# Performance work log

Hardware: AMD Instinct MI355X
Metric: run time of the kernel (lower is better)

Reference implementation:

```python
import jax, jax.numpy as jnp
import numpy as np

N, E = 50000, 800000
NODE_DIM, EDGE_DIM, HID, OUT = 128, 16, 256, 32
NEG_SLOPE = 0.2


def setup_inputs() -> dict:
    key = jax.random.key(0)
    ks = jax.random.split(key, 20)
    def p(k, shape, fan_in):
        return jax.random.normal(k, shape, dtype=jnp.float32) * (1.0 / np.sqrt(fan_in))
    inp = {
        'x': jax.random.normal(ks[0], (N, NODE_DIM), dtype=jnp.float32),
        'edge_index': jax.random.randint(ks[1], (2, E), 0, N, dtype=jnp.int32),
        'edge_attr': jax.random.normal(ks[2], (E, EDGE_DIM), dtype=jnp.float32),
        # layer 1: GATv2Conv(node_dim -> 256, edge_dim)
        'Wl1': p(ks[3], (NODE_DIM, HID), NODE_DIM), 'bl1': jnp.zeros((HID,), jnp.float32),
        'Wr1': p(ks[4], (NODE_DIM, HID), NODE_DIM), 'br1': jnp.zeros((HID,), jnp.float32),
        'We1': p(ks[5], (EDGE_DIM, HID), EDGE_DIM),
        'att1': p(ks[6], (HID,), HID), 'bias1': jnp.zeros((HID,), jnp.float32),
        # layer 2: GATv2Conv(256 -> 32, edge_dim)
        'Wl2': p(ks[7], (HID, OUT), HID), 'bl2': jnp.zeros((OUT,), jnp.float32),
        'Wr2': p(ks[8], (HID, OUT), HID), 'br2': jnp.zeros((OUT,), jnp.float32),
        'We2': p(ks[9], (EDGE_DIM, OUT), EDGE_DIM),
        'att2': p(ks[10], (OUT,), OUT), 'bias2': jnp.zeros((OUT,), jnp.float32),
    }
    return inp


def _gatv2_layer(x, src, dst, ea, Wl, bl, Wr, br, We, att, bias, n_nodes):
    # GATv2: e_ij = att . leaky_relu(Wl x_j + Wr x_i + We e_ij), softmax over j for each target i
    xl = x @ Wl + bl            # [N, C] source transform
    xr = x @ Wr + br            # [N, C] target transform
    ee = ea @ We                # [Etot, C]
    z = jax.nn.leaky_relu(xl[src] + xr[dst] + ee, NEG_SLOPE)  # [Etot, C]
    e = z @ att                 # [Etot]
    m = jax.ops.segment_max(e, dst, num_segments=n_nodes)
    m = jnp.where(jnp.isfinite(m), m, 0.0)
    a = jnp.exp(e - m[dst])
    s = jax.ops.segment_sum(a, dst, num_segments=n_nodes)
    alpha = a / (s[dst] + 1e-16)
    out = jax.ops.segment_sum(alpha[:, None] * xl[src], dst, num_segments=n_nodes)
    return out + bias


def reference(x, edge_index, edge_attr, Wl1, bl1, Wr1, br1, We1, att1, bias1,
              Wl2, bl2, Wr2, br2, We2, att2, bias2):
    n = x.shape[0]
    src, dst = edge_index[0], edge_index[1]
    # add_self_loops with fill_value='mean': self-loop attr = mean of incoming edge_attr
    deg = jax.ops.segment_sum(jnp.ones((src.shape[0],), x.dtype), dst, num_segments=n)
    loop_attr = jax.ops.segment_sum(edge_attr, dst, num_segments=n) / jnp.maximum(deg, 1.0)[:, None]
    ar = jnp.arange(n, dtype=src.dtype)
    src_a = jnp.concatenate([src, ar])
    dst_a = jnp.concatenate([dst, ar])
    ea = jnp.concatenate([edge_attr, loop_attr], axis=0)
    h = _gatv2_layer(x, src_a, dst_a, ea, Wl1, bl1, Wr1, br1, We1, att1, bias1, n)
    h = _gatv2_layer(h, src_a, dst_a, ea, Wl2, bl2, Wr2, br2, We2, att2, bias2, n)
    return h.mean(0)  # [OUT]
```

## Files before the change

kernel.cpp:

```cpp
#include <hip/hip_runtime.h>
#include <hip/hip_bf16.h>
#include <stdint.h>


#define NN 50000
#define NE 800000
#define DIN 128
#define DE 16
#define HID 256
#define OUTD 32
#define SLOPE 0.2f
#define CAP 64
#define FILLBLKS 3125

__global__ __launch_bounds__(256) void k_fill_xform1(
    const int* __restrict__ srcv, const int* __restrict__ dstv,
    int* __restrict__ deg, int2* __restrict__ es,
    const float* __restrict__ x, const float* __restrict__ Wl,
    const float* __restrict__ bl, const float* __restrict__ Wr,
    const float* __restrict__ br, float* __restrict__ xl, float* __restrict__ xr) {
  const int bid = blockIdx.x;
  if (bid < FILLBLKS) {
    int e = bid * 256 + threadIdx.x;
    if (e < NE) {
      int d = dstv[e];
      int p = atomicAdd(&deg[d], 1);
      if (p < CAP) es[(size_t)d * CAP + p] = make_int2(e, srcv[e]);
    }
    return;
  }
  const int c = threadIdx.x;
  const int r0 = (bid - FILLBLKS) * 16;
  float accl[16], accr[16];
#pragma unroll
  for (int r = 0; r < 16; ++r) { accl[r] = 0.f; accr[r] = 0.f; }
  const float* __restrict__ xb = x + (size_t)r0 * DIN;
#pragma unroll 4
  for (int k = 0; k < DIN; ++k) {
    const float wl = Wl[k * HID + c];
    const float wr = Wr[k * HID + c];
#pragma unroll
    for (int r = 0; r < 16; ++r) {
      const float xv = xb[r * DIN + k];
      accl[r] = fmaf(xv, wl, accl[r]);
      accr[r] = fmaf(xv, wr, accr[r]);
    }
  }
  const float blc = bl[c], brc = br[c];
#pragma unroll
  for (int r = 0; r < 16; ++r) {
    xl[(size_t)(r0 + r) * HID + c] = accl[r] + blc;
    xr[(size_t)(r0 + r) * HID + c] = accr[r] + brc;
  }
}


__global__ __launch_bounds__(256) void k_loopattr(
    const float* __restrict__ ea, const int* __restrict__ degv,
    const int2* __restrict__ es, float* __restrict__ loopat) {
  const int tid = threadIdx.x;
  const int lane = tid & 63;
  const int wid = tid >> 6;
  const int node = blockIdx.x * 4 + wid;
  const int grp = lane >> 4;
  const int ch = lane & 15;
  const int deg = degv[node];
  const int r0 = node * CAP, r1 = r0 + deg;

  float acc = 0.f;
  for (int j = r0 + grp; j < r1; j += 4) {
    const int e = es[j].x;
    acc += ea[(size_t)e * DE + ch];
  }
  acc += __shfl_xor(acc, 16, 64);
  acc += __shfl_xor(acc, 32, 64);
  if (grp == 0) {
    const float invd = 1.f / (float)(deg > 0 ? deg : 1);
    loopat[(size_t)node * DE + ch] = acc * invd;
  }
}


__global__ __launch_bounds__(256)
__attribute__((amdgpu_num_vgpr(64))) void k_edge1(
    const float* __restrict__ xl, const float* __restrict__ xr,
    const float* __restrict__ eattr, const float* __restrict__ loopat,
    const int* __restrict__ degv, const int2* __restrict__ es,
    const float* __restrict__ We, const float* __restrict__ att,
    const float* __restrict__ bias, float* __restrict__ hout) {
  const int tid = threadIdx.x;
  const int lane = tid & 63;
  const int wid = tid >> 6;
  const int node = blockIdx.x * 4 + wid;
  const int c0 = lane << 2;

  float we[DE][4];
#pragma unroll
  for (int k = 0; k < DE; ++k) {
    const float4 w4 = *(const float4*)(We + k * HID + c0);
    we[k][0] = w4.x; we[k][1] = w4.y; we[k][2] = w4.z; we[k][3] = w4.w;
  }
  const float4 attv = *(const float4*)(att + c0);
  const float4 xrv = *(const float4*)(xr + (size_t)node * HID + c0);
  const int r0 = node * CAP;
  const int r1 = r0 + degv[node];

  float ssum = 0.f;
  float a0 = 0.f, a1 = 0.f, a2 = 0.f, a3 = 0.f;

  auto pscore = [&](const float* __restrict__ eap, const float4 xs) -> float {
    const float4* __restrict__ eb = (const float4*)eap;
    const float4 A0 = eb[0], A1 = eb[1], A2 = eb[2], A3 = eb[3];
    float e0, e1, e2, e3;
    e0 = A0.x * we[0][0]; e1 = A0.x * we[0][1];
    e2 = A0.x * we[0][2]; e3 = A0.x * we[0][3];
    e0 = fmaf(A0.y, we[1][0], e0); e1 = fmaf(A0.y, we[1][1], e1);
    e2 = fmaf(A0.y, we[1][2], e2); e3 = fmaf(A0.y, we[1][3], e3);
    e0 = fmaf(A0.z, we[2][0], e0); e1 = fmaf(A0.z, we[2][1], e1);
    e2 = fmaf(A0.z, we[2][2], e2); e3 = fmaf(A0.z, we[2][3], e3);
    e0 = fmaf(A0.w, we[3][0], e0); e1 = fmaf(A0.w, we[3][1], e1);
    e2 = fmaf(A0.w, we[3][2], e2); e3 = fmaf(A0.w, we[3][3], e3);
    e0 = fmaf(A1.x, we[4][0], e0); e1 = fmaf(A1.x, we[4][1], e1);
    e2 = fmaf(A1.x, we[4][2], e2); e3 = fmaf(A1.x, we[4][3], e3);
    e0 = fmaf(A1.y, we[5][0], e0); e1 = fmaf(A1.y, we[5][1], e1);
    e2 = fmaf(A1.y, we[5][2], e2); e3 = fmaf(A1.y, we[5][3], e3);
    e0 = fmaf(A1.z, we[6][0], e0); e1 = fmaf(A1.z, we[6][1], e1);
    e2 = fmaf(A1.z, we[6][2], e2); e3 = fmaf(A1.z, we[6][3], e3);
    e0 = fmaf(A1.w, we[7][0], e0); e1 = fmaf(A1.w, we[7][1], e1);
    e2 = fmaf(A1.w, we[7][2], e2); e3 = fmaf(A1.w, we[7][3], e3);
    e0 = fmaf(A2.x, we[8][0], e0); e1 = fmaf(A2.x, we[8][1], e1);
    e2 = fmaf(A2.x, we[8][2], e2); e3 = fmaf(A2.x, we[8][3], e3);
    e0 = fmaf(A2.y, we[9][0], e0); e1 = fmaf(A2.y, we[9][1], e1);
    e2 = fmaf(A2.y, we[9][2], e2); e3 = fmaf(A2.y, we[9][3], e3);
    e0 = fmaf(A2.z, we[10][0], e0); e1 = fmaf(A2.z, we[10][1], e1);
    e2 = fmaf(A2.z, we[10][2], e2); e3 = fmaf(A2.z, we[10][3], e3);
    e0 = fmaf(A2.w, we[11][0], e0); e1 = fmaf(A2.w, we[11][1], e1);
    e2 = fmaf(A2.w, we[11][2], e2); e3 = fmaf(A2.w, we[11][3], e3);
    e0 = fmaf(A3.x, we[12][0], e0); e1 = fmaf(A3.x, we[12][1], e1);
    e2 = fmaf(A3.x, we[12][2], e2); e3 = fmaf(A3.x, we[12][3], e3);
    e0 = fmaf(A3.y, we[13][0], e0); e1 = fmaf(A3.y, we[13][1], e1);
    e2 = fmaf(A3.y, we[13][2], e2); e3 = fmaf(A3.y, we[13][3], e3);
    e0 = fmaf(A3.z, we[14][0], e0); e1 = fmaf(A3.z, we[14][1], e1);
    e2 = fmaf(A3.z, we[14][2], e2); e3 = fmaf(A3.z, we[14][3], e3);
    e0 = fmaf(A3.w, we[15][0], e0); e1 = fmaf(A3.w, we[15][1], e1);
    e2 = fmaf(A3.w, we[15][2], e2); e3 = fmaf(A3.w, we[15][3], e3);
    float z0 = xs.x + xrv.x + e0;
    float z1 = xs.y + xrv.y + e1;
    float z2 = xs.z + xrv.z + e2;
    float z3 = xs.w + xrv.w + e3;
    z0 = fmaxf(z0, SLOPE * z0);
    z1 = fmaxf(z1, SLOPE * z1);
    z2 = fmaxf(z2, SLOPE * z2);
    z3 = fmaxf(z3, SLOPE * z3);
    float p = z0 * attv.x;
    p = fmaf(z1, attv.y, p);
    p = fmaf(z2, attv.z, p);
    p = fmaf(z3, attv.w, p);
    return p;
  };

  auto upd = [&](float p, const float4 xs) {
    const float w = __expf(p);
    ssum += w;
    a0 = fmaf(w, xs.x, a0);
    a1 = fmaf(w, xs.y, a1);
    a2 = fmaf(w, xs.z, a2);
    a3 = fmaf(w, xs.w, a3);
  };

  int j = r0;
  for (; j + 4 <= r1; j += 4) {
    const int2 q0 = es[j], q1 = es[j + 1], q2 = es[j + 2], q3 = es[j + 3];
    const int s0i = __builtin_amdgcn_readfirstlane(q0.y);
    const int s1i = __builtin_amdgcn_readfirstlane(q1.y);
    const int s2i = __builtin_amdgcn_readfirstlane(q2.y);
    const int s3i = __builtin_amdgcn_readfirstlane(q3.y);
    const int e0i = __builtin_amdgcn_readfirstlane(q0.x);
    const int e1i = __builtin_amdgcn_readfirstlane(q1.x);
    const int e2i = __builtin_amdgcn_readfirstlane(q2.x);
    const int e3i = __builtin_amdgcn_readfirstlane(q3.x);
    const float4 xs0 = *(const float4*)(xl + (size_t)s0i * HID + c0);
    const float4 xs1 = *(const float4*)(xl + (size_t)s1i * HID + c0);
    const float4 xs2 = *(const float4*)(xl + (size_t)s2i * HID + c0);
    const float4 xs3 = *(const float4*)(xl + (size_t)s3i * HID + c0);
    float p0 = pscore(eattr + (size_t)e0i * DE, xs0);
    float p1 = pscore(eattr + (size_t)e1i * DE, xs1);
    float p2 = pscore(eattr + (size_t)e2i * DE, xs2);
    float p3 = pscore(eattr + (size_t)e3i * DE, xs3);
#pragma unroll
    for (int off = 32; off >= 1; off >>= 1) {
      p0 += __shfl_xor(p0, off, 64);
      p1 += __shfl_xor(p1, off, 64);
      p2 += __shfl_xor(p2, off, 64);
      p3 += __shfl_xor(p3, off, 64);
    }
    upd(p0, xs0);
    upd(p1, xs1);
    upd(p2, xs2);
    upd(p3, xs3);
  }
  for (; j < r1; ++j) {
    const int2 q = es[j];
    const int ei = __builtin_amdgcn_readfirstlane(q.x);
    const int si = __builtin_amdgcn_readfirstlane(q.y);
    const float4 xs = *(const float4*)(xl + (size_t)si * HID + c0);
    float p = pscore(eattr + (size_t)ei * DE, xs);
#pragma unroll
    for (int off = 32; off >= 1; off >>= 1) p += __shfl_xor(p, off, 64);
    upd(p, xs);
  }

  {
    const float4 xs = *(const float4*)(xl + (size_t)node * HID + c0);
    float p = pscore(loopat + (size_t)node * DE, xs);
#pragma unroll
    for (int off = 32; off >= 1; off >>= 1) p += __shfl_xor(p, off, 64);
    upd(p, xs);
  }

  const float inv = 1.f / (ssum + 1e-16f);
  const float4 bv = *(const float4*)(bias + c0);
  float4 o;
  o.x = fmaf(a0, inv, bv.x);
  o.y = fmaf(a1, inv, bv.y);
  o.z = fmaf(a2, inv, bv.z);
  o.w = fmaf(a3, inv, bv.w);
  *(float4*)(hout + (size_t)node * HID + c0) = o;
}


__global__ __launch_bounds__(256) void k_xform2(const float* __restrict__ h,
                                                const float* __restrict__ Wl,
                                                const float* __restrict__ bl,
                                                const float* __restrict__ Wr,
                                                const float* __restrict__ br,
                                                float* __restrict__ xl2,
                                                float* __restrict__ xr2) {
  const int t = threadIdx.x;
  const int c = t & 63;
  const int wv = t >> 6;
  const int cc = c & 31;
  const int r0 = blockIdx.x * 32 + wv * 8;
  const float* __restrict__ Wp = (c < 32) ? Wl : Wr;
  const float* __restrict__ bp = (c < 32) ? bl : br;
  float* __restrict__ op = (c < 32) ? xl2 : xr2;

  int rr[8];
#pragma unroll
  for (int i = 0; i < 8; ++i) {
    int r = r0 + i;
    rr[i] = r < NN ? r : NN - 1;
  }
  float acc[8];
#pragma unroll
  for (int i = 0; i < 8; ++i) acc[i] = 0.f;
#pragma unroll 4
  for (int k = 0; k < HID; ++k) {
    const float wval = Wp[k * OUTD + cc];
#pragma unroll
    for (int i = 0; i < 8; ++i) {
      acc[i] = fmaf(h[(size_t)rr[i] * HID + k], wval, acc[i]);
    }
  }
  const float bb = bp[cc];
#pragma unroll
  for (int i = 0; i < 8; ++i) {
    int r = r0 + i;
    if (r < NN) op[(size_t)r * OUTD + cc] = acc[i] + bb;
  }
}


__global__ __launch_bounds__(256, 4) void k_edge2(
    const float* __restrict__ xl2, const float* __restrict__ xr2,
    const float* __restrict__ eattr, const float* __restrict__ loopat,
    const int* __restrict__ degv, const int2* __restrict__ es,
    const float* __restrict__ We2, const float* __restrict__ att2,
    float* __restrict__ partials) {
  __shared__ float sacc[OUTD];
  const int tid = threadIdx.x;
  const int lane = tid & 63;
  const int wid = tid >> 6;
  const int half = lane >> 5;
  const int node = blockIdx.x * 8 + wid * 2 + half;
  const int c = lane & 31;

  if (tid < OUTD) sacc[tid] = 0.f;
  __syncthreads();

  float we2[DE];
#pragma unroll
  for (int k = 0; k < DE; ++k) we2[k] = We2[k * OUTD + c];
  const float attc = att2[c];
  const float xrc = xr2[(size_t)node * OUTD + c];
  const int r0 = node * CAP;
  const int r1 = r0 + degv[node];

  float ssum = 0.f, acc = 0.f;

  auto eecalc = [&](const float* __restrict__ ap) -> float {
    const float4* __restrict__ eb = (const float4*)ap;
    const float4 A0 = eb[0], A1 = eb[1], A2 = eb[2], A3 = eb[3];
    float ee = A0.x * we2[0];
    ee = fmaf(A0.y, we2[1], ee);
    ee = fmaf(A0.z, we2[2], ee);
    ee = fmaf(A0.w, we2[3], ee);
    ee = fmaf(A1.x, we2[4], ee);
    ee = fmaf(A1.y, we2[5], ee);
    ee = fmaf(A1.z, we2[6], ee);
    ee = fmaf(A1.w, we2[7], ee);
    ee = fmaf(A2.x, we2[8], ee);
    ee = fmaf(A2.y, we2[9], ee);
    ee = fmaf(A2.z, we2[10], ee);
    ee = fmaf(A2.w, we2[11], ee);
    ee = fmaf(A3.x, we2[12], ee);
    ee = fmaf(A3.y, we2[13], ee);
    ee = fmaf(A3.z, we2[14], ee);
    ee = fmaf(A3.w, we2[15], ee);
    return ee;
  };
  auto pfin = [&](float xs, float ee) -> float {
    float z = xs + xrc + ee;
    z = fmaxf(z, SLOPE * z);
    return z * attc;
  };
  auto upd = [&](float p, float xs) {
    const float w = __expf(p);
    ssum += w;
    acc = fmaf(w, xs, acc);
  };

  int j = r0;
  for (; j + 8 <= r1; j += 8) {
    int2 q[8];
#pragma unroll
    for (int u = 0; u < 8; ++u) q[u] = es[j + u];
    float xs[8], ee[8], p[8];
#pragma unroll
    for (int u = 0; u < 8; ++u) xs[u] = xl2[(size_t)q[u].y * OUTD + c];
#pragma unroll
    for (int u = 0; u < 8; ++u) ee[u] = eecalc(eattr + (size_t)q[u].x * DE);
#pragma unroll
    for (int u = 0; u < 8; ++u) p[u] = pfin(xs[u], ee[u]);
#pragma unroll
    for (int off = 16; off >= 1; off >>= 1) {
#pragma unroll
      for (int u = 0; u < 8; ++u) p[u] += __shfl_xor(p[u], off, 64);
    }
#pragma unroll
    for (int u = 0; u < 8; ++u) upd(p[u], xs[u]);
  }
  for (; j + 2 <= r1; j += 2) {
    const int2 qa = es[j], qb = es[j + 1];
    const float xsa = xl2[(size_t)qa.y * OUTD + c];
    const float xsb = xl2[(size_t)qb.y * OUTD + c];
    const float eea = eecalc(eattr + (size_t)qa.x * DE);
    const float eeb = eecalc(eattr + (size_t)qb.x * DE);
    float pa = pfin(xsa, eea);
    float pb = pfin(xsb, eeb);
#pragma unroll
    for (int off = 16; off >= 1; off >>= 1) {
      pa += __shfl_xor(pa, off, 64);
      pb += __shfl_xor(pb, off, 64);
    }
    upd(pa, xsa);
    upd(pb, xsb);
  }
  for (; j < r1; ++j) {
    const int2 q = es[j];
    const float xs = xl2[(size_t)q.y * OUTD + c];
    const float ee = eecalc(eattr + (size_t)q.x * DE);
    float p = pfin(xs, ee);
#pragma unroll
    for (int off = 16; off >= 1; off >>= 1) p += __shfl_xor(p, off, 64);
    upd(p, xs);
  }

  {
    const float xs = xl2[(size_t)node * OUTD + c];
    const float ee = eecalc(loopat + (size_t)node * DE);
    float p = pfin(xs, ee);
#pragma unroll
    for (int off = 16; off >= 1; off >>= 1) p += __shfl_xor(p, off, 64);
    upd(p, xs);
  }

  const float h2 = acc / (ssum + 1e-16f);
  atomicAdd(&sacc[c], h2);
  __syncthreads();
  if (tid < OUTD) partials[(size_t)blockIdx.x * OUTD + tid] = sacc[tid];
}


__global__ __launch_bounds__(256) void k_final(const float* __restrict__ partials,
                                               const float* __restrict__ bias2,
                                               float* __restrict__ out, int nblk) {
  __shared__ float lds[256];
  const int cch = blockIdx.x;
  const int t = threadIdx.x;
  float s = 0.f;
  for (int b = t; b < nblk; b += 256) s += partials[(size_t)b * OUTD + cch];
  lds[t] = s;
  __syncthreads();
  for (int off = 128; off >= 1; off >>= 1) {
    if (t < off) lds[t] += lds[t + off];
    __syncthreads();
  }
  if (t == 0) out[cch] = lds[0] * (1.f / (float)NN) + bias2[cch];
}


static inline size_t alup(size_t x) { return (x + 255) & ~(size_t)255; }

extern "C" void kernel_launch(void* const* d_in, const int* in_sizes, int n_in,
                              void* d_out, int out_size, void* d_ws, size_t ws_size,
                              hipStream_t stream) {
  (void)in_sizes; (void)n_in; (void)out_size; (void)ws_size;
  const float* x = (const float*)d_in[0];
  const int* ei = (const int*)d_in[1];
  const float* ea = (const float*)d_in[2];
  const float* Wl1 = (const float*)d_in[3];
  const float* bl1 = (const float*)d_in[4];
  const float* Wr1 = (const float*)d_in[5];
  const float* br1 = (const float*)d_in[6];
  const float* We1 = (const float*)d_in[7];
  const float* att1 = (const float*)d_in[8];
  const float* bias1 = (const float*)d_in[9];
  const float* Wl2 = (const float*)d_in[10];
  const float* bl2 = (const float*)d_in[11];
  const float* Wr2 = (const float*)d_in[12];
  const float* br2 = (const float*)d_in[13];
  const float* We2 = (const float*)d_in[14];
  const float* att2 = (const float*)d_in[15];
  const float* bias2 = (const float*)d_in[16];
  const int* srcv = ei;
  const int* dstv = ei + NE;

  char* w = (char*)d_ws;
  int* deg = (int*)w;        w += alup((size_t)NN * 4);
  int2* es = (int2*)w;       w += alup((size_t)NN * CAP * 8);
  float* loopat = (float*)w; w += alup((size_t)NN * DE * 4);
  float* xl1 = (float*)w;    w += alup((size_t)NN * HID * 4);
  float* xr1 = (float*)w;    w += alup((size_t)NN * HID * 4);
  float* h = (float*)w;      w += alup((size_t)NN * HID * 4);
  float* partials = (float*)w;
  float* xl2 = xl1;
  float* xr2 = xr1;

  float* out = (float*)d_out;
  const int nblkNode4 = NN / 4;
  const int nblkNode8 = NN / 8;

  hipMemsetAsync(deg, 0, (size_t)NN * 4, stream);

  k_fill_xform1<<<FILLBLKS + NN / 16, 256, 0, stream>>>(
      srcv, dstv, deg, es, x, Wl1, bl1, Wr1, br1, xl1, xr1);
  k_loopattr<<<nblkNode4, 256, 0, stream>>>(ea, deg, es, loopat);
  k_edge1<<<nblkNode4, 256, 0, stream>>>(xl1, xr1, ea, loopat, deg, es,
                                         We1, att1, bias1, h);
  k_xform2<<<(NN + 31) / 32, 256, 0, stream>>>(h, Wl2, bl2, Wr2, br2, xl2, xr2);
  k_edge2<<<nblkNode8, 256, 0, stream>>>(xl2, xr2, ea, loopat, deg, es,
                                         We2, att2, partials);
  k_final<<<OUTD, 256, 0, stream>>>(partials, bias2, out, nblkNode8);
}
```

Before: 576.9 us.

## Derive self-loop edge term from running sum of projected edge features

Removes the separate loop-attribute kernel and its buffer. Because the projection We is linear, the self-loop's projected edge term equals the mean of the projected incoming edge terms. Both edge kernels therefore accumulate the projected values they already compute and divide by the degree. This saves a kernel launch and a gather pass over edge_attr, at the cost of a few extra accumulator registers in k_edge1, which is capped at 64 VGPRs. Summing in a different order may change the floating-point result slightly.

```diff
diff --git a/kernel.cpp b/kernel.cpp
--- a/kernel.cpp
+++ b/kernel.cpp
@@ -55,39 +55,13 @@
 }
 
 
-__global__ __launch_bounds__(256) void k_loopattr(
-    const float* __restrict__ ea, const int* __restrict__ degv,
-    const int2* __restrict__ es, float* __restrict__ loopat) {
-  const int tid = threadIdx.x;
-  const int lane = tid & 63;
-  const int wid = tid >> 6;
-  const int node = blockIdx.x * 4 + wid;
-  const int grp = lane >> 4;
-  const int ch = lane & 15;
-  const int deg = degv[node];
-  const int r0 = node * CAP, r1 = r0 + deg;
-
-  float acc = 0.f;
-  for (int j = r0 + grp; j < r1; j += 4) {
-    const int e = es[j].x;
-    acc += ea[(size_t)e * DE + ch];
-  }
-  acc += __shfl_xor(acc, 16, 64);
-  acc += __shfl_xor(acc, 32, 64);
-  if (grp == 0) {
-    const float invd = 1.f / (float)(deg > 0 ? deg : 1);
-    loopat[(size_t)node * DE + ch] = acc * invd;
-  }
-}
-
-
 __global__ __launch_bounds__(256)
 __attribute__((amdgpu_num_vgpr(64))) void k_edge1(
     const float* __restrict__ xl, const float* __restrict__ xr,
-    const float* __restrict__ eattr, const float* __restrict__ loopat,
-    const int* __restrict__ degv, const int2* __restrict__ es,
-    const float* __restrict__ We, const float* __restrict__ att,
-    const float* __restrict__ bias, float* __restrict__ hout) {
+    const float* __restrict__ eattr, const int* __restrict__ degv,
+    const int2* __restrict__ es, const float* __restrict__ We,
+    const float* __restrict__ att, const float* __restrict__ bias,
+    float* __restrict__ hout) {
   const int tid = threadIdx.x;
   const int lane = tid & 63;
   const int wid = tid >> 6;
@@ -102,16 +76,18 @@
   }
   const float4 attv = *(const float4*)(att + c0);
   const float4 xrv = *(const float4*)(xr + (size_t)node * HID + c0);
+  const int deg = degv[node];
   const int r0 = node * CAP;
-  const int r1 = r0 + degv[node];
+  const int r1 = r0 + deg;
 
   float ssum = 0.f;
   float a0 = 0.f, a1 = 0.f, a2 = 0.f, a3 = 0.f;
-
-  auto pscore = [&](const float* __restrict__ eap, const float4 xs) -> float {
-    const float4* __restrict__ eb = (const float4*)eap;
+  float s0 = 0.f, s1 = 0.f, s2 = 0.f, s3 = 0.f;
+
+  auto eecalc = [&](const float* __restrict__ ap, float& e0, float& e1,
+                    float& e2, float& e3) {
+    const float4* __restrict__ eb = (const float4*)ap;
     const float4 A0 = eb[0], A1 = eb[1], A2 = eb[2], A3 = eb[3];
-    float e0, e1, e2, e3;
     e0 = A0.x * we[0][0]; e1 = A0.x * we[0][1];
     e2 = A0.x * we[0][2]; e3 = A0.x * we[0][3];
     e0 = fmaf(A0.y, we[1][0], e0); e1 = fmaf(A0.y, we[1][1], e1);
@@ -144,6 +120,9 @@
     e2 = fmaf(A3.z, we[14][2], e2); e3 = fmaf(A3.z, we[14][3], e3);
     e0 = fmaf(A3.w, we[15][0], e0); e1 = fmaf(A3.w, we[15][1], e1);
     e2 = fmaf(A3.w, we[15][2], e2); e3 = fmaf(A3.w, we[15][3], e3);
+  };
+  auto pfin = [&](const float4 xs, float e0, float e1, float e2,
+                  float e3) -> float {
     float z0 = xs.x + xrv.x + e0;
     float z1 = xs.y + xrv.y + e1;
     float z2 = xs.z + xrv.z + e2;
@@ -158,7 +137,6 @@
     p = fmaf(z3, attv.w, p);
     return p;
   };
-
   auto upd = [&](float p, const float4 xs) {
     const float w = __expf(p);
     ssum += w;
@@ -183,10 +161,20 @@
     const float4 xs1 = *(const float4*)(xl + (size_t)s1i * HID + c0);
     const float4 xs2 = *(const float4*)(xl + (size_t)s2i * HID + c0);
     const float4 xs3 = *(const float4*)(xl + (size_t)s3i * HID + c0);
-    float p0 = pscore(eattr + (size_t)e0i * DE, xs0);
-    float p1 = pscore(eattr + (size_t)e1i * DE, xs1);
-    float p2 = pscore(eattr + (size_t)e2i * DE, xs2);
-    float p3 = pscore(eattr + (size_t)e3i * DE, xs3);
+    float e00, e01, e02, e03, e10, e11, e12, e13;
+    float e20, e21, e22, e23, e30, e31, e32, e33;
+    eecalc(eattr + (size_t)e0i * DE, e00, e01, e02, e03);
+    eecalc(eattr + (size_t)e1i * DE, e10, e11, e12, e13);
+    eecalc(eattr + (size_t)e2i * DE, e20, e21, e22, e23);
+    eecalc(eattr + (size_t)e3i * DE, e30, e31, e32, e33);
+    s0 += (e00 + e10) + (e20 + e30);
+    s1 += (e01 + e11) + (e21 + e31);
+    s2 += (e02 + e12) + (e22 + e32);
+    s3 += (e03 + e13) + (e23 + e33);
+    float p0 = pfin(xs0, e00, e01, e02, e03);
+    float p1 = pfin(xs1, e10, e11, e12, e13);
+    float p2 = pfin(xs2, e20, e21, e22, e23);
+    float p3 = pfin(xs3, e30, e31, e32, e33);
 #pragma unroll
     for (int off = 32; off >= 1; off >>= 1) {
       p0 += __shfl_xor(p0, off, 64);
@@ -204,15 +192,19 @@
     const int ei = __builtin_amdgcn_readfirstlane(q.x);
     const int si = __builtin_amdgcn_readfirstlane(q.y);
     const float4 xs = *(const float4*)(xl + (size_t)si * HID + c0);
-    float p = pscore(eattr + (size_t)ei * DE, xs);
+    float e0, e1, e2, e3;
+    eecalc(eattr + (size_t)ei * DE, e0, e1, e2, e3);
+    s0 += e0; s1 += e1; s2 += e2; s3 += e3;
+    float p = pfin(xs, e0, e1, e2, e3);
 #pragma unroll
     for (int off = 32; off >= 1; off >>= 1) p += __shfl_xor(p, off, 64);
     upd(p, xs);
   }
 
   {
+    const float invd = 1.f / (float)(deg > 0 ? deg : 1);
     const float4 xs = *(const float4*)(xl + (size_t)node * HID + c0);
-    float p = pscore(loopat + (size_t)node * DE, xs);
+    float p = pfin(xs, s0 * invd, s1 * invd, s2 * invd, s3 * invd);
 #pragma unroll
     for (int off = 32; off >= 1; off >>= 1) p += __shfl_xor(p, off, 64);
     upd(p, xs);
@@ -273,10 +265,9 @@
 
 __global__ __launch_bounds__(256, 4) void k_edge2(
     const float* __restrict__ xl2, const float* __restrict__ xr2,
-    const float* __restrict__ eattr, const float* __restrict__ loopat,
-    const int* __restrict__ degv, const int2* __restrict__ es,
-    const float* __restrict__ We2, const float* __restrict__ att2,
-    float* __restrict__ partials) {
+    const float* __restrict__ eattr, const int* __restrict__ degv,
+    const int2* __restrict__ es, const float* __restrict__ We2,
+    const float* __restrict__ att2, float* __restrict__ partials) {
   __shared__ float sacc[OUTD];
   const int tid = threadIdx.x;
   const int lane = tid & 63;
@@ -293,10 +284,11 @@
   for (int k = 0; k < DE; ++k) we2[k] = We2[k * OUTD + c];
   const float attc = att2[c];
   const float xrc = xr2[(size_t)node * OUTD + c];
+  const int deg = degv[node];
   const int r0 = node * CAP;
-  const int r1 = r0 + degv[node];
-
-  float ssum = 0.f, acc = 0.f;
+  const int r1 = r0 + deg;
+
+  float ssum = 0.f, acc = 0.f, see = 0.f;
 
   auto eecalc = [&](const float* __restrict__ ap) -> float {
     const float4* __restrict__ eb = (const float4*)ap;
@@ -341,6 +333,8 @@
 #pragma unroll
     for (int u = 0; u < 8; ++u) ee[u] = eecalc(eattr + (size_t)q[u].x * DE);
 #pragma unroll
+    for (int u = 0; u < 8; ++u) see += ee[u];
+#pragma unroll
     for (int u = 0; u < 8; ++u) p[u] = pfin(xs[u], ee[u]);
 #pragma unroll
     for (int off = 16; off >= 1; off >>= 1) {
@@ -356,6 +350,7 @@
     const float xsb = xl2[(size_t)qb.y * OUTD + c];
     const float eea = eecalc(eattr + (size_t)qa.x * DE);
     const float eeb = eecalc(eattr + (size_t)qb.x * DE);
+    see += eea + eeb;
     float pa = pfin(xsa, eea);
     float pb = pfin(xsb, eeb);
 #pragma unroll
@@ -370,6 +365,7 @@
     const int2 q = es[j];
     const float xs = xl2[(size_t)q.y * OUTD + c];
     const float ee = eecalc(eattr + (size_t)q.x * DE);
+    see += ee;
     float p = pfin(xs, ee);
 #pragma unroll
     for (int off = 16; off >= 1; off >>= 1) p += __shfl_xor(p, off, 64);
@@ -377,9 +373,9 @@
   }
 
   {
+    const float invd = 1.f / (float)(deg > 0 ? deg : 1);
     const float xs = xl2[(size_t)node * OUTD + c];
-    const float ee = eecalc(loopat + (size_t)node * DE);
-    float p = pfin(xs, ee);
+    float p = pfin(xs, see * invd);
 #pragma unroll
     for (int off = 16; off >= 1; off >>= 1) p += __shfl_xor(p, off, 64);
     upd(p, xs);
@@ -439,7 +435,6 @@
   char* w = (char*)d_ws;
   int* deg = (int*)w;        w += alup((size_t)NN * 4);
   int2* es = (int2*)w;       w += alup((size_t)NN * CAP * 8);
-  float* loopat = (float*)w; w += alup((size_t)NN * DE * 4);
   float* xl1 = (float*)w;    w += alup((size_t)NN * HID * 4);
   float* xr1 = (float*)w;    w += alup((size_t)NN * HID * 4);
   float* h = (float*)w;      w += alup((size_t)NN * HID * 4);
@@ -455,11 +450,10 @@
 
   k_fill_xform1<<<FILLBLKS + NN / 16, 256, 0, stream>>>(
       srcv, dstv, deg, es, x, Wl1, bl1, Wr1, br1, xl1, xr1);
-  k_loopattr<<<nblkNode4, 256, 0, stream>>>(ea, deg, es, loopat);
-  k_edge1<<<nblkNode4, 256, 0, stream>>>(xl1, xr1, ea, loopat, deg, es,
+  k_edge1<<<nblkNode4, 256, 0, stream>>>(xl1, xr1, ea, deg, es,
                                          We1, att1, bias1, h);
   k_xform2<<<(NN + 31) / 32, 256, 0, stream>>>(h, Wl2, bl2, Wr2, br2, xl2, xr2);
-  k_edge2<<<nblkNode8, 256, 0, stream>>>(xl2, xr2, ea, loopat, deg, es,
+  k_edge2<<<nblkNode8, 256, 0, stream>>>(xl2, xr2, ea, deg, es,
                                          We2, att2, partials);
   k_final<<<OUTD, 256, 0, stream>>>(partials, bias2, out, nblkNode8);
 }
```

After: 1.796 ms. +211.3%, slower.
